# Kernel optimization log

Measured on AMD Instinct MI355X. Metric: run time of the kernel, lower is better.

## Reference

```python
import jax, jax.numpy as jnp
import numpy as np

B = 4096          # batch size (scaled up from source's 16)
INPUT_AXIS = 784
LATENT_DIM = 2


def _pdist(x):
    # pairwise euclidean distances in itertools.combinations order (row-major upper triangle)
    sq = jnp.sum(x * x, axis=1)                      # [B]
    d2 = sq[:, None] + sq[None, :] - 2.0 * (x @ x.T)  # [B,B]
    i, j = jnp.triu_indices(x.shape[0], k=1)
    return jnp.sqrt(jnp.maximum(d2[i, j], 0.0))       # [B*(B-1)/2]


def setup_inputs() -> dict:
    key = jax.random.key(0)
    ks = jax.random.split(key, 17)
    dims = [(400, 784), (200, 400), (50, 200), (2, 50),
            (50, 2), (200, 50), (400, 200), (784, 400)]
    names = ['fc1', 'fc1_1', 'fc1_2', 'fc2', 'fc3', 'fc3_1', 'fc3_2', 'fc4']
    inp = {'x': jax.random.uniform(ks[0], (B, 1, 28, 28), dtype=jnp.float32)}
    for idx, (nm, (o, i)) in enumerate(zip(names, dims)):
        bound = 1.0 / np.sqrt(i)
        inp[nm + '_w'] = jax.random.uniform(ks[1 + 2 * idx], (o, i), jnp.float32, -bound, bound)
        inp[nm + '_b'] = jax.random.uniform(ks[2 + 2 * idx], (o,), jnp.float32, -bound, bound)
    return inp


def reference(x, fc1_w, fc1_b, fc1_1_w, fc1_1_b, fc1_2_w, fc1_2_b, fc2_w, fc2_b,
              fc3_w, fc3_b, fc3_1_w, fc3_1_b, fc3_2_w, fc3_2_b, fc4_w, fc4_b):
    lin = lambda h, w, b: h @ w.T + b
    lrelu = jax.nn.leaky_relu  # default slope 0.01, matches F.leaky_relu
    x2 = x.reshape(-1, INPUT_AXIS)                       # [B,784]
    h = lrelu(lin(x2, fc1_w, fc1_b))
    h = lrelu(lin(h, fc1_1_w, fc1_1_b))
    h = lrelu(lin(h, fc1_2_w, fc1_2_b))                  # encoder out [B,50]
    z = lin(jnp.tanh(h), fc2_w, fc2_b)                   # [B,2]
    y = lrelu(lin(z, fc3_w, fc3_b))
    y = lrelu(lin(y, fc3_1_w, fc3_1_b))
    y = lrelu(lin(y, fc3_2_w, fc3_2_b))
    y = jax.nn.sigmoid(lin(y, fc4_w, fc4_b))             # [B,784]
    y_img = y.reshape(B, 1, 28, 28)
    in_diff = _pdist(x2)
    lat_diff = _pdist(z)
    out_diff = _pdist(y.reshape(B, INPUT_AXIS))
    return (y_img, in_diff, lat_diff, out_diff, z)
```

## Files before the change

kernel.cpp:

```cpp
#include <hip/hip_runtime.h>
#include <math.h>

#define NB 4096
#define DIMX 784

typedef __attribute__((ext_vector_type(8))) short bf16x8;
typedef __attribute__((ext_vector_type(4))) float f32x4;

__device__ __forceinline__ float lrelu_f(float v) { return v >= 0.f ? v : 0.01f * v; }

__device__ __forceinline__ void split1(float x, short& hi_s, short& lo_s) {
    unsigned u = __float_as_uint(x);
    unsigned hib = (u + 0x7FFFu + ((u >> 16) & 1u)) & 0xFFFF0000u;
    float hif = __uint_as_float(hib);
    float lo = x - hif;
    unsigned ul = __float_as_uint(lo);
    unsigned lob = (ul + 0x7FFFu + ((ul >> 16) & 1u)) >> 16;
    hi_s = (short)(hib >> 16);
    lo_s = (short)lob;
}

#define GLL(srcp, dstp) __builtin_amdgcn_global_load_lds( \
    (const __attribute__((address_space(1))) void*)(srcp), \
    (__attribute__((address_space(3))) void*)(dstp), 16, 0, 0)


__global__ __launch_bounds__(256) void prep_all(
    const float* __restrict__ w1, const float* __restrict__ w11,
    const float* __restrict__ w32, const float* __restrict__ w4,
    short* __restrict__ o1, short* __restrict__ o11,
    short* __restrict__ o32, short* __restrict__ o4,
    const float* __restrict__ X, short* __restrict__ Xs,
    float* __restrict__ sqx, float* __restrict__ sqy)
{
    const int bid = blockIdx.x;
    const int t = threadIdx.x;
    if (bid < 3920) {
        const float* W; short* O; int N, K, NP, KP, base;
        if (bid < 1600)      { W = w1;  O = o1;  N = 400; K = 784; NP = 512; KP = 800; base = 0; }
        else if (bid < 2016) { W = w11; O = o11; N = 200; K = 400; NP = 256; KP = 416; base = 1600; }
        else if (bid < 2464) { W = w32; O = o32; N = 400; K = 200; NP = 512; KP = 224; base = 2016; }
        else                 { W = w4;  O = o4;  N = 784; K = 400; NP = 896; KP = 416; base = 2464; }
        const int idx = (bid - base) * 256 + t;
        if (idx >= NP * KP) return;
        const int r = idx / KP, k = idx - r * KP;
        short hi = 0, lo = 0;
        if (r < N && k < K) split1(W[(size_t)r * K + k], hi, lo);
        O[(size_t)r * 2 * KP + k]      = hi;
        O[(size_t)r * 2 * KP + KP + k] = lo;
    } else {
        const int r = bid - 3920;
        float s = 0.f;
        if (t < 200) {
            const int k0 = t * 4;
            short h[4] = {0, 0, 0, 0}, l[4] = {0, 0, 0, 0};
            if (k0 < 784) {
                float4 v = *(const float4*)(X + (size_t)r * 784 + k0);
                split1(v.x, h[0], l[0]); split1(v.y, h[1], l[1]);
                split1(v.z, h[2], l[2]); split1(v.w, h[3], l[3]);
                s = v.x * v.x + v.y * v.y + v.z * v.z + v.w * v.w;
            }
            *(uint2*)&Xs[(size_t)r * 1600 + k0]       = *(const uint2*)h;
            *(uint2*)&Xs[(size_t)r * 1600 + 800 + k0] = *(const uint2*)l;
        }
        __shared__ float red[256];
        red[t] = s;
        __syncthreads();
        for (int off = 128; off > 0; off >>= 1) {
            if (t < off) red[t] += red[t + off];
            __syncthreads();
        }
        if (t == 0) { sqx[r] = red[0]; sqy[r] = 0.f; }
    }
}

template<int ACT, bool WF32, bool WSPLIT, bool WROWSQ>
__global__ __launch_bounds__(256) void gemm3_64(
    const short* __restrict__ As_g, const short* __restrict__ Ws_g,
    const float* __restrict__ bias, float* __restrict__ C,
    short* __restrict__ Cs, int N, int KPi, int nchunk, int KPo,
    float* __restrict__ sqy)
{
    __shared__ short L[2][12288];
    const int tid = threadIdx.x;
    const int w = tid >> 6, lane = tid & 63;
    const int wc = w;
    const int m0 = blockIdx.y * 64, n0 = blockIdx.x * 128;
    const int frow = lane & 15;
    const int fk_sw = (((lane >> 4) ^ ((lane >> 1) & 3))) * 8;
    const int srow = tid >> 2;
    const int scol_sw = (((tid & 3) ^ ((tid >> 3) & 3))) * 8;
    const int RS = 2 * KPi;
    const int ld0 = w * 512;

    const short* gA  = As_g + (size_t)(m0 + srow) * RS + scol_sw;
    const short* gB0 = Ws_g + (size_t)(n0 + srow) * RS + scol_sw;
    const short* gB1 = gB0 + (size_t)64 * RS;

    f32x4 acc[4][2] = {};

    auto stage = [&](int buf, int km) {
        GLL(gA  + km,       &L[buf][ld0]);
        GLL(gA  + KPi + km, &L[buf][2048 + ld0]);
        GLL(gB0 + km,       &L[buf][4096 + ld0]);
        GLL(gB1 + km,       &L[buf][6144 + ld0]);
        GLL(gB0 + KPi + km, &L[buf][8192 + ld0]);
        GLL(gB1 + KPi + km, &L[buf][10240 + ld0]);
    };

    stage(0, 0);
    asm volatile("s_waitcnt vmcnt(0)" ::: "memory");
    __builtin_amdgcn_s_barrier();
    int buf = 0;
    #pragma unroll 1
    for (int cc = 0; cc < nchunk; ++cc) {
        if (cc + 1 < nchunk) {
            stage(buf ^ 1, (cc + 1) * 32);
            asm volatile("s_waitcnt vmcnt(6)" ::: "memory");
        } else {
            asm volatile("s_waitcnt vmcnt(0)" ::: "memory");
        }
        __builtin_amdgcn_s_barrier();

        bf16x8 ah[4], al[4], bh[2], bl[2];
        #pragma unroll
        for (int m = 0; m < 4; ++m) {
            const int ro = (m * 16 + frow) * 32 + fk_sw;
            ah[m] = *(const bf16x8*)&L[buf][ro];
            al[m] = *(const bf16x8*)&L[buf][2048 + ro];
        }
        #pragma unroll
        for (int n = 0; n < 2; ++n) {
            const int ro = (wc * 32 + n * 16 + frow) * 32 + fk_sw;
            bh[n] = *(const bf16x8*)&L[buf][4096 + ro];
            bl[n] = *(const bf16x8*)&L[buf][8192 + ro];
        }
        __builtin_amdgcn_s_setprio(1);
        #pragma unroll
        for (int m = 0; m < 4; ++m)
            #pragma unroll
            for (int n = 0; n < 2; ++n) {
                acc[m][n] = __builtin_amdgcn_mfma_f32_16x16x32_bf16(ah[m], bh[n], acc[m][n], 0, 0, 0);
                acc[m][n] = __builtin_amdgcn_mfma_f32_16x16x32_bf16(ah[m], bl[n], acc[m][n], 0, 0, 0);
                acc[m][n] = __builtin_amdgcn_mfma_f32_16x16x32_bf16(al[m], bh[n], acc[m][n], 0, 0, 0);
            }
        __builtin_amdgcn_s_setprio(0);
        __builtin_amdgcn_s_barrier();
        buf ^= 1;
    }

    const int col0 = lane & 15;
    const int row4 = (lane >> 4) * 4;

    float* rowsum = (float*)&L[0][0];
    if (WROWSQ) {
        __syncthreads();
        if (tid < 64) rowsum[tid] = 0.f;
        __syncthreads();
    }

    #pragma unroll
    for (int m = 0; m < 4; ++m) {
        #pragma unroll
        for (int r = 0; r < 4; ++r) {
            const int gm = m0 + m * 16 + row4 + r;
            float vsq = 0.f;
            #pragma unroll
            for (int n = 0; n < 2; ++n) {
                const int gn = n0 + wc * 32 + n * 16 + col0;
                float v = 0.f;
                if (gn < N) {
                    v = acc[m][n][r] + bias[gn];
                    if (ACT == 1)      v = lrelu_f(v);
                    else if (ACT == 2) v = 1.f / (1.f + expf(-v));
                }
                if (WF32 && gn < N) C[(size_t)gm * N + gn] = v;
                if (WSPLIT && gn < KPo) {
                    short hi, lo; split1(v, hi, lo);
                    Cs[(size_t)gm * 2 * KPo + gn]       = hi;
                    Cs[(size_t)gm * 2 * KPo + KPo + gn] = lo;
                }
                if (WROWSQ) vsq = fmaf(v, v, vsq);
            }
            if (WROWSQ) atomicAdd(&rowsum[m * 16 + row4 + r], vsq);
        }
    }
    if (WROWSQ) {
        __syncthreads();
        if (tid < 64) atomicAdd(&sqy[m0 + tid], rowsum[tid]);
    }
}

__global__ __launch_bounds__(256) void fused_mid(
    const float* __restrict__ h2, const float* __restrict__ W12,
    const float* __restrict__ b12, const float* __restrict__ W2,
    const float* __restrict__ b2,  const float* __restrict__ W3,
    const float* __restrict__ b3,  const float* __restrict__ W31,
    const float* __restrict__ b31, float* __restrict__ z_out,
    short* __restrict__ y2s)
{
    __shared__ float wbuf[200 * 51];
    __shared__ float hl[16 * 201];
    __shared__ float h3l[16 * 51];
    __shared__ float y1l[16 * 51];
    __shared__ float zl[16 * 2];
    __shared__ float w2l[100], w3l[100];
    __shared__ float b12l[50], b2l[2], b3l[50], b31l[200];
    const int t = threadIdx.x;
    const int r0 = blockIdx.x * 16;

    for (int i = t; i < 50 * 200; i += 256) { int n = i / 200, k = i - n * 200; wbuf[n * 201 + k] = W12[i]; }
    for (int i = t; i < 16 * 200; i += 256) { int r = i / 200, k = i - r * 200; hl[r * 201 + k] = h2[(size_t)(r0 + r) * 200 + k]; }
    for (int i = t; i < 100; i += 256) { w2l[i] = W2[i]; w3l[i] = W3[i]; }
    if (t < 50)  { b12l[t] = b12[t]; b3l[t] = b3[t]; }
    if (t < 2)   b2l[t] = b2[t];
    if (t < 200) b31l[t] = b31[t];
    __syncthreads();

    for (int i = t; i < 16 * 50; i += 256) {
        int r = i / 50, n = i - r * 50;
        float s = b12l[n];
        #pragma unroll 4
        for (int k = 0; k < 200; ++k) s = fmaf(hl[r * 201 + k], wbuf[n * 201 + k], s);
        h3l[r * 51 + n] = tanhf(lrelu_f(s));
    }
    __syncthreads();

    if (t < 32) {
        int r = t >> 1, n = t & 1;
        float s = b2l[n];
        #pragma unroll
        for (int k = 0; k < 50; ++k) s = fmaf(h3l[r * 51 + k], w2l[n * 50 + k], s);
        zl[r * 2 + n] = s;
        z_out[(size_t)(r0 + r) * 2 + n] = s;
    }
    for (int i = t; i < 200 * 50; i += 256) { int n = i / 50, k = i - n * 50; wbuf[n * 51 + k] = W31[i]; }
    __syncthreads();

    for (int i = t; i < 16 * 50; i += 256) {
        int r = i / 50, n = i - r * 50;
        float s = fmaf(zl[r * 2], w3l[n * 2], fmaf(zl[r * 2 + 1], w3l[n * 2 + 1], b3l[n]));
        y1l[r * 51 + n] = lrelu_f(s);
    }
    __syncthreads();

    for (int i = t; i < 16 * 224; i += 256) {
        int r = i / 224, n = i - r * 224;
        float v = 0.f;
        if (n < 200) {
            float s = b31l[n];
            #pragma unroll
            for (int k = 0; k < 50; ++k) s = fmaf(y1l[r * 51 + k], wbuf[n * 51 + k], s);
            v = lrelu_f(s);
        }
        short hi, lo; split1(v, hi, lo);
        const size_t gm = r0 + r;
        y2s[gm * 448 + n]       = hi;
        y2s[gm * 448 + 224 + n] = lo;
    }
}

__global__ __launch_bounds__(256, 4) void pdist_all(
    const short* __restrict__ xs, const short* __restrict__ ys,
    const float* __restrict__ sqx, const float* __restrict__ sqy,
    const float* __restrict__ Z, float* __restrict__ in_diff,
    float* __restrict__ out_diff, float* __restrict__ lat_diff)
{
    __shared__ short L[4][4096];
    const int tid = threadIdx.x;
    const int orig = blockIdx.x;

    if (orig < 528) {
        const int b = (orig & 7) * 66 + (orig >> 3);
        int rem = b, ti = 0;
        while (rem >= 32 - ti) { rem -= 32 - ti; ++ti; }
        const int tj = ti + rem;

        const int w = tid >> 6, lane = tid & 63;
        const int wr = w >> 1, wc = w & 1;
        const int frow = lane & 15;
        const int fk_sw = (((lane >> 4) ^ ((lane >> 1) & 3))) * 8;
        const int srow = tid >> 2;
        const int scol_sw = (((tid & 3) ^ ((tid >> 3) & 3))) * 8;
        const int i0 = ti * 128, j0 = tj * 128;
        const int ld0 = w * 512;

        const short* gA = ys + (size_t)(i0 + srow) * 1600 + scol_sw;
        const short* gB = ys + (size_t)(j0 + srow) * 1600 + scol_sw;
        const size_t half = (size_t)64 * 1600;

        f32x4 acc[4][4] = {};

        #pragma unroll 1
        for (int cc = 0; cc < 25; ++cc) {
            const int km = cc * 32;
            __syncthreads();
            GLL(gA + km,       &L[0][ld0]);   GLL(gA + half + km,       &L[0][2048 + ld0]);
            GLL(gB + km,       &L[2][ld0]);   GLL(gB + half + km,       &L[2][2048 + ld0]);
            GLL(gA + 800 + km, &L[1][ld0]);   GLL(gA + half + 800 + km, &L[1][2048 + ld0]);
            GLL(gB + 800 + km, &L[3][ld0]);   GLL(gB + half + 800 + km, &L[3][2048 + ld0]);
            __syncthreads();

            bf16x8 ah[4], bh[4];
            #pragma unroll
            for (int m = 0; m < 4; ++m)
                ah[m] = *(const bf16x8*)&L[0][(wr * 64 + m * 16 + frow) * 32 + fk_sw];
            #pragma unroll
            for (int n = 0; n < 4; ++n)
                bh[n] = *(const bf16x8*)&L[2][(wc * 64 + n * 16 + frow) * 32 + fk_sw];
            __builtin_amdgcn_s_setprio(1);
            #pragma unroll
            for (int m = 0; m < 4; ++m)
                #pragma unroll
                for (int n = 0; n < 4; ++n)
                    acc[m][n] = __builtin_amdgcn_mfma_f32_16x16x32_bf16(ah[m], bh[n], acc[m][n], 0, 0, 0);

            bf16x8 al[4], bl[4];
            #pragma unroll
            for (int n = 0; n < 4; ++n)
                bl[n] = *(const bf16x8*)&L[3][(wc * 64 + n * 16 + frow) * 32 + fk_sw];
            #pragma unroll
            for (int m = 0; m < 4; ++m)
                #pragma unroll
                for (int n = 0; n < 4; ++n)
                    acc[m][n] = __builtin_amdgcn_mfma_f32_16x16x32_bf16(ah[m], bl[n], acc[m][n], 0, 0, 0);
            #pragma unroll
            for (int m = 0; m < 4; ++m)
                al[m] = *(const bf16x8*)&L[1][(wr * 64 + m * 16 + frow) * 32 + fk_sw];
            #pragma unroll
            for (int m = 0; m < 4; ++m)
                #pragma unroll
                for (int n = 0; n < 4; ++n)
                    acc[m][n] = __builtin_amdgcn_mfma_f32_16x16x32_bf16(al[m], bh[n], acc[m][n], 0, 0, 0);
            __builtin_amdgcn_s_setprio(0);
        }

        const int col0 = lane & 15;
        const int row4 = (lane >> 4) * 4;
        float sqj_v[4];
        #pragma unroll
        for (int n = 0; n < 4; ++n)
            sqj_v[n] = sqy[j0 + wc * 64 + n * 16 + col0];

        #pragma unroll
        for (int m = 0; m < 4; ++m) {
            #pragma unroll
            for (int r = 0; r < 4; ++r) {
                const int gi = i0 + wr * 64 + m * 16 + row4 + r;
                const float sqi = sqy[gi];
                const int rowbase = (gi * (2 * NB - 1 - gi)) / 2 - gi - 1;
                #pragma unroll
                for (int n = 0; n < 4; ++n) {
                    const int gj = j0 + wc * 64 + n * 16 + col0;
                    if (gj > gi) {
                        float d2 = sqi + sqj_v[n] - 2.f * acc[m][n][r];
                        out_diff[rowbase + gj] = sqrtf(fmaxf(d2, 0.f));
                    }
                }
            }
        }
    } else if (orig < 1056) {
        const int o = orig - 528;
        const int b = (o & 7) * 66 + (o >> 3);
        int rem = b, ti = 0;
        while (rem >= 32 - ti) { rem -= 32 - ti; ++ti; }
        const int tj = ti + rem;

        const int w = tid >> 6, lane = tid & 63;
        const int wr = w >> 1, wc = w & 1;
        const int frow = lane & 15;
        const int fk_sw = (((lane >> 4) ^ ((lane >> 1) & 3))) * 8;
        const int srow = tid >> 2;
        const int scol_sw = (((tid & 3) ^ ((tid >> 3) & 3))) * 8;
        const int i0 = ti * 128, j0 = tj * 128;
        const int ld0 = w * 512;

        const short* gA = xs + (size_t)(i0 + srow) * 1600 + scol_sw;
        const short* gB = xs + (size_t)(j0 + srow) * 1600 + scol_sw;
        const size_t half = (size_t)64 * 1600;

        f32x4 acc[4][4] = {};

        auto stage = [&](int buf, int km) {
            short* dA = buf ? &L[2][0] : &L[0][0];
            short* dB = buf ? &L[3][0] : &L[1][0];
            GLL(gA + km,        dA + ld0);   GLL(gA + half + km, dA + 2048 + ld0);
            GLL(gB + km,        dB + ld0);   GLL(gB + half + km, dB + 2048 + ld0);
        };

        stage(0, 0);
        asm volatile("s_waitcnt vmcnt(0)" ::: "memory");
        __builtin_amdgcn_s_barrier();
        int buf = 0;
        #pragma unroll 1
        for (int cc = 0; cc < 25; ++cc) {
            if (cc < 24) {
                stage(buf ^ 1, (cc + 1) * 32);
                asm volatile("s_waitcnt vmcnt(4)" ::: "memory");
            } else {
                asm volatile("s_waitcnt vmcnt(0)" ::: "memory");
            }
            __builtin_amdgcn_s_barrier();

            const short* SA = buf ? &L[2][0] : &L[0][0];
            const short* SB = buf ? &L[3][0] : &L[1][0];
            bf16x8 a[4], bb[4];
            #pragma unroll
            for (int m = 0; m < 4; ++m)
                a[m] = *(const bf16x8*)&SA[(wr * 64 + m * 16 + frow) * 32 + fk_sw];
            #pragma unroll
            for (int n = 0; n < 4; ++n)
                bb[n] = *(const bf16x8*)&SB[(wc * 64 + n * 16 + frow) * 32 + fk_sw];
            __builtin_amdgcn_s_setprio(1);
            #pragma unroll
            for (int m = 0; m < 4; ++m)
                #pragma unroll
                for (int n = 0; n < 4; ++n)
                    acc[m][n] = __builtin_amdgcn_mfma_f32_16x16x32_bf16(a[m], bb[n], acc[m][n], 0, 0, 0);
            __builtin_amdgcn_s_setprio(0);
            __builtin_amdgcn_s_barrier();
            buf ^= 1;
        }

        const int col0 = lane & 15;
        const int row4 = (lane >> 4) * 4;
        float sqj_v[4];
        #pragma unroll
        for (int n = 0; n < 4; ++n)
            sqj_v[n] = sqx[j0 + wc * 64 + n * 16 + col0];
        #pragma unroll
        for (int m = 0; m < 4; ++m) {
            #pragma unroll
            for (int r = 0; r < 4; ++r) {
                const int gi = i0 + wr * 64 + m * 16 + row4 + r;
                const float sqi = sqx[gi];
                const int rowbase = (gi * (2 * NB - 1 - gi)) / 2 - gi - 1;
                #pragma unroll
                for (int n = 0; n < 4; ++n) {
                    const int gj = j0 + wc * 64 + n * 16 + col0;
                    if (gj > gi) {
                        float d2 = sqi + sqj_v[n] - 2.f * acc[m][n][r];
                        in_diff[rowbase + gj] = sqrtf(fmaxf(d2, 0.f));
                    }
                }
            }
        }
    } else {
        const int o = orig - 1056;
        const int b = (o & 7) * 66 + (o >> 3);
        int rem = b, ti = 0;
        while (rem >= 32 - ti) { rem -= 32 - ti; ++ti; }
        const int tj = ti + rem;
        const int i0 = ti * 128, j0 = tj * 128;

        float* zi = (float*)&L[0][0];
        float* zj = (float*)&L[0][512];
        if (tid < 128) {
            *(float2*)&zi[tid * 2] = *(const float2*)&Z[(size_t)(i0 + tid) * 2];
        } else {
            const int r = tid - 128;
            *(float2*)&zj[r * 2] = *(const float2*)&Z[(size_t)(j0 + r) * 2];
        }
        __syncthreads();

        const int ty = tid >> 4;
        const int tx = tid & 15;
        #pragma unroll
        for (int ii = 0; ii < 8; ++ii) {
            const int li = ty * 8 + ii;
            const int gi = i0 + li;
            const int rowbase = (gi * (2 * NB - 1 - gi)) / 2 - gi - 1;
            const float zi0 = zi[li * 2], zi1 = zi[li * 2 + 1];
            #pragma unroll
            for (int jj = 0; jj < 8; ++jj) {
                const int lj = tx * 8 + jj;
                const int gj = j0 + lj;
                if (gj > gi) {
                    float d0 = zi0 - zj[lj * 2];
                    float d1 = zi1 - zj[lj * 2 + 1];
                    lat_diff[rowbase + gj] = sqrtf(fmaf(d0, d0, d1 * d1));
                }
            }
        }
    }
}

extern "C" void kernel_launch(void* const* d_in, const int* in_sizes, int n_in,
                              void* d_out, int out_size, void* d_ws, size_t ws_size,
                              hipStream_t stream)
{
    const float* x       = (const float*)d_in[0];
    const float* fc1_w   = (const float*)d_in[1];
    const float* fc1_b   = (const float*)d_in[2];
    const float* fc11_w  = (const float*)d_in[3];
    const float* fc11_b  = (const float*)d_in[4];
    const float* fc12_w  = (const float*)d_in[5];
    const float* fc12_b  = (const float*)d_in[6];
    const float* fc2_w   = (const float*)d_in[7];
    const float* fc2_b   = (const float*)d_in[8];
    const float* fc3_w   = (const float*)d_in[9];
    const float* fc3_b   = (const float*)d_in[10];
    const float* fc31_w  = (const float*)d_in[11];
    const float* fc31_b  = (const float*)d_in[12];
    const float* fc32_w  = (const float*)d_in[13];
    const float* fc32_b  = (const float*)d_in[14];
    const float* fc4_w   = (const float*)d_in[15];
    const float* fc4_b   = (const float*)d_in[16];

    float* out = (float*)d_out;
    float* y        = out;
    float* in_diff  = out + 3211264;
    float* lat_diff = out + 11597824;
    float* out_diff = out + 19984384;
    float* z        = out + 28370944;

    float* ws   = (float*)d_ws;
    float* h2   = ws;
    float* h3u  = h2  + (size_t)4096 * 200;
    float* y1u  = h3u + (size_t)4096 * 50;
    float* sqx  = y1u + (size_t)4096 * 50;
    float* sqy  = sqx + 4096;
    short* xs   = (short*)(sqy + 4096);
    short* ys   = xs  + (size_t)NB * 1600;
    short* w1s  = ys  + (size_t)NB * 1600;
    short* w11s = w1s  + (size_t)512 * 1600;
    short* w32s = w11s + (size_t)256 * 832;
    short* w4s  = w32s + (size_t)512 * 448;
    short* h1s  = w4s  + (size_t)896 * 832;
    short* y3s  = h1s;
    short* y2s  = h1s  + (size_t)4096 * 832;

    const dim3 blk(256);

    prep_all<<<dim3(8016), blk, 0, stream>>>(
        fc1_w, fc11_w, fc32_w, fc4_w, w1s, w11s, w32s, w4s, x, xs, sqx, sqy);
    gemm3_64<1, false, true, false><<<dim3(4, 64), blk, 0, stream>>>(
        xs, w1s, fc1_b, nullptr, h1s, 400, 800, 25, 416, nullptr);
    gemm3_64<1, true, false, false><<<dim3(2, 64), blk, 0, stream>>>(
        h1s, w11s, fc11_b, h2, nullptr, 200, 416, 13, 0, nullptr);
    fused_mid<<<dim3(256), blk, 0, stream>>>(
        h2, fc12_w, fc12_b, fc2_w, fc2_b, fc3_w, fc3_b, fc31_w, fc31_b, z, y2s);
    gemm3_64<1, false, true, false><<<dim3(4, 64), blk, 0, stream>>>(
        y2s, w32s, fc32_b, nullptr, y3s, 400, 224, 7, 416, nullptr);
    gemm3_64<2, true, true, true><<<dim3(7, 64), blk, 0, stream>>>(
        y3s, w4s, fc4_b, y, ys, 784, 416, 13, 800, sqy);
    pdist_all<<<dim3(1584), blk, 0, stream>>>(
        xs, ys, sqx, sqy, z, in_diff, out_diff, lat_diff);
}
```

Baseline: 225.8 us.

## Compute output pairwise distances from bf16 high parts only, sharing the input-distance path

The fc4 GEMM now writes only the bf16 high half of y, with an 800-wide row stride, when HIONLY is set. The out_diff pairwise-distance tiles reuse the single-pass path already used for in_diff, replacing the three-pass hi/lo split-bf16 MFMA path. Row squared norms for both x and y are now computed from the rounded high parts, so they match the bf16 dot products. This cuts MFMA work and memory traffic for the output distances to about a third, at the cost of lower precision in out_diff.

```diff
diff --git a/kernel.cpp b/kernel.cpp
--- a/kernel.cpp
+++ b/kernel.cpp
@@ -9,7 +9,7 @@
 
 __device__ __forceinline__ float lrelu_f(float v) { return v >= 0.f ? v : 0.01f * v; }
 
-__device__ __forceinline__ void split1(float x, short& hi_s, short& lo_s) {
+__device__ __forceinline__ float split1h(float x, short& hi_s, short& lo_s) {
     unsigned u = __float_as_uint(x);
     unsigned hib = (u + 0x7FFFu + ((u >> 16) & 1u)) & 0xFFFF0000u;
     float hif = __uint_as_float(hib);
@@ -18,6 +18,7 @@
     unsigned lob = (ul + 0x7FFFu + ((ul >> 16) & 1u)) >> 16;
     hi_s = (short)(hib >> 16);
     lo_s = (short)lob;
+    return hif;
 }
 
 #define GLL(srcp, dstp) __builtin_amdgcn_global_load_lds( \
@@ -45,7 +46,7 @@
         if (idx >= NP * KP) return;
         const int r = idx / KP, k = idx - r * KP;
         short hi = 0, lo = 0;
-        if (r < N && k < K) split1(W[(size_t)r * K + k], hi, lo);
+        if (r < N && k < K) split1h(W[(size_t)r * K + k], hi, lo);
         O[(size_t)r * 2 * KP + k]      = hi;
         O[(size_t)r * 2 * KP + KP + k] = lo;
     } else {
@@ -56,9 +57,11 @@
             short h[4] = {0, 0, 0, 0}, l[4] = {0, 0, 0, 0};
             if (k0 < 784) {
                 float4 v = *(const float4*)(X + (size_t)r * 784 + k0);
-                split1(v.x, h[0], l[0]); split1(v.y, h[1], l[1]);
-                split1(v.z, h[2], l[2]); split1(v.w, h[3], l[3]);
-                s = v.x * v.x + v.y * v.y + v.z * v.z + v.w * v.w;
+                float h0 = split1h(v.x, h[0], l[0]);
+                float h1 = split1h(v.y, h[1], l[1]);
+                float h2v = split1h(v.z, h[2], l[2]);
+                float h3v = split1h(v.w, h[3], l[3]);
+                s = h0 * h0 + h1 * h1 + h2v * h2v + h3v * h3v;
             }
             *(uint2*)&Xs[(size_t)r * 1600 + k0]       = *(const uint2*)h;
             *(uint2*)&Xs[(size_t)r * 1600 + 800 + k0] = *(const uint2*)l;
@@ -74,7 +77,7 @@
     }
 }
 
-template<int ACT, bool WF32, bool WSPLIT, bool WROWSQ>
+template<int ACT, bool WF32, bool WSPLIT, bool WROWSQ, bool HIONLY>
 __global__ __launch_bounds__(256) void gemm3_64(
     const short* __restrict__ As_g, const short* __restrict__ Ws_g,
     const float* __restrict__ bias, float* __restrict__ C,
@@ -176,11 +179,16 @@
                 }
                 if (WF32 && gn < N) C[(size_t)gm * N + gn] = v;
                 if (WSPLIT && gn < KPo) {
-                    short hi, lo; split1(v, hi, lo);
-                    Cs[(size_t)gm * 2 * KPo + gn]       = hi;
-                    Cs[(size_t)gm * 2 * KPo + KPo + gn] = lo;
+                    short hi, lo;
+                    float hif = split1h(v, hi, lo);
+                    if (HIONLY) {
+                        Cs[(size_t)gm * KPo + gn] = hi;
+                    } else {
+                        Cs[(size_t)gm * 2 * KPo + gn]       = hi;
+                        Cs[(size_t)gm * 2 * KPo + KPo + gn] = lo;
+                    }
+                    if (WROWSQ) vsq = fmaf(hif, hif, vsq);
                 }
-                if (WROWSQ) vsq = fmaf(v, v, vsq);
             }
             if (WROWSQ) atomicAdd(&rowsum[m * 16 + row4 + r], vsq);
         }
@@ -253,7 +261,8 @@
             for (int k = 0; k < 50; ++k) s = fmaf(y1l[r * 51 + k], wbuf[n * 51 + k], s);
             v = lrelu_f(s);
         }
-        short hi, lo; split1(v, hi, lo);
+        short hi, lo;
+        split1h(v, hi, lo);
         const size_t gm = r0 + r;
         y2s[gm * 448 + n]       = hi;
         y2s[gm * 448 + 224 + n] = lo;
@@ -270,11 +279,18 @@
     const int tid = threadIdx.x;
     const int orig = blockIdx.x;
 
-    if (orig < 528) {
-        const int b = (orig & 7) * 66 + (orig >> 3);
+    if (orig < 1056) {
+        const bool isY = (orig < 528);
+        const int o = isY ? orig : orig - 528;
+        const int b = (o & 7) * 66 + (o >> 3);
         int rem = b, ti = 0;
         while (rem >= 32 - ti) { rem -= 32 - ti; ++ti; }
         const int tj = ti + rem;
+
+        const short* Xs = isY ? ys : xs;
+        const int rs    = isY ? 800 : 1600;
+        const float* sq = isY ? sqy : sqx;
+        float* outp     = isY ? out_diff : in_diff;
 
         const int w = tid >> 6, lane = tid & 63;
         const int wr = w >> 1, wc = w & 1;
@@ -285,99 +301,9 @@
         const int i0 = ti * 128, j0 = tj * 128;
         const int ld0 = w * 512;
 
-        const short* gA = ys + (size_t)(i0 + srow) * 1600 + scol_sw;
-        const short* gB = ys + (size_t)(j0 + srow) * 1600 + scol_sw;
-        const size_t half = (size_t)64 * 1600;
-
-        f32x4 acc[4][4] = {};
-
-        #pragma unroll 1
-        for (int cc = 0; cc < 25; ++cc) {
-            const int km = cc * 32;
-            __syncthreads();
-            GLL(gA + km,       &L[0][ld0]);   GLL(gA + half + km,       &L[0][2048 + ld0]);
-            GLL(gB + km,       &L[2][ld0]);   GLL(gB + half + km,       &L[2][2048 + ld0]);
-            GLL(gA + 800 + km, &L[1][ld0]);   GLL(gA + half + 800 + km, &L[1][2048 + ld0]);
-            GLL(gB + 800 + km, &L[3][ld0]);   GLL(gB + half + 800 + km, &L[3][2048 + ld0]);
-            __syncthreads();
-
-            bf16x8 ah[4], bh[4];
-            #pragma unroll
-            for (int m = 0; m < 4; ++m)
-                ah[m] = *(const bf16x8*)&L[0][(wr * 64 + m * 16 + frow) * 32 + fk_sw];
-            #pragma unroll
-            for (int n = 0; n < 4; ++n)
-                bh[n] = *(const bf16x8*)&L[2][(wc * 64 + n * 16 + frow) * 32 + fk_sw];
-            __builtin_amdgcn_s_setprio(1);
-            #pragma unroll
-            for (int m = 0; m < 4; ++m)
-                #pragma unroll
-                for (int n = 0; n < 4; ++n)
-                    acc[m][n] = __builtin_amdgcn_mfma_f32_16x16x32_bf16(ah[m], bh[n], acc[m][n], 0, 0, 0);
-
-            bf16x8 al[4], bl[4];
-            #pragma unroll
-            for (int n = 0; n < 4; ++n)
-                bl[n] = *(const bf16x8*)&L[3][(wc * 64 + n * 16 + frow) * 32 + fk_sw];
-            #pragma unroll
-            for (int m = 0; m < 4; ++m)
-                #pragma unroll
-                for (int n = 0; n < 4; ++n)
-                    acc[m][n] = __builtin_amdgcn_mfma_f32_16x16x32_bf16(ah[m], bl[n], acc[m][n], 0, 0, 0);
-            #pragma unroll
-            for (int m = 0; m < 4; ++m)
-                al[m] = *(const bf16x8*)&L[1][(wr * 64 + m * 16 + frow) * 32 + fk_sw];
-            #pragma unroll
-            for (int m = 0; m < 4; ++m)
-                #pragma unroll
-                for (int n = 0; n < 4; ++n)
-                    acc[m][n] = __builtin_amdgcn_mfma_f32_16x16x32_bf16(al[m], bh[n], acc[m][n], 0, 0, 0);
-            __builtin_amdgcn_s_setprio(0);
-        }
-
-        const int col0 = lane & 15;
-        const int row4 = (lane >> 4) * 4;
-        float sqj_v[4];
-        #pragma unroll
-        for (int n = 0; n < 4; ++n)
-            sqj_v[n] = sqy[j0 + wc * 64 + n * 16 + col0];
-
-        #pragma unroll
-        for (int m = 0; m < 4; ++m) {
-            #pragma unroll
-            for (int r = 0; r < 4; ++r) {
-                const int gi = i0 + wr * 64 + m * 16 + row4 + r;
-                const float sqi = sqy[gi];
-                const int rowbase = (gi * (2 * NB - 1 - gi)) / 2 - gi - 1;
-                #pragma unroll
-                for (int n = 0; n < 4; ++n) {
-                    const int gj = j0 + wc * 64 + n * 16 + col0;
-                    if (gj > gi) {
-                        float d2 = sqi + sqj_v[n] - 2.f * acc[m][n][r];
-                        out_diff[rowbase + gj] = sqrtf(fmaxf(d2, 0.f));
-                    }
-                }
-            }
-        }
-    } else if (orig < 1056) {
-        const int o = orig - 528;
-        const int b = (o & 7) * 66 + (o >> 3);
-        int rem = b, ti = 0;
-        while (rem >= 32 - ti) { rem -= 32 - ti; ++ti; }
-        const int tj = ti + rem;
-
-        const int w = tid >> 6, lane = tid & 63;
-        const int wr = w >> 1, wc = w & 1;
-        const int frow = lane & 15;
-        const int fk_sw = (((lane >> 4) ^ ((lane >> 1) & 3))) * 8;
-        const int srow = tid >> 2;
-        const int scol_sw = (((tid & 3) ^ ((tid >> 3) & 3))) * 8;
-        const int i0 = ti * 128, j0 = tj * 128;
-        const int ld0 = w * 512;
-
-        const short* gA = xs + (size_t)(i0 + srow) * 1600 + scol_sw;
-        const short* gB = xs + (size_t)(j0 + srow) * 1600 + scol_sw;
-        const size_t half = (size_t)64 * 1600;
+        const short* gA = Xs + (size_t)(i0 + srow) * rs + scol_sw;
+        const short* gB = Xs + (size_t)(j0 + srow) * rs + scol_sw;
+        const size_t half = (size_t)64 * rs;
 
         f32x4 acc[4][4] = {};
 
@@ -427,20 +353,20 @@
         float sqj_v[4];
         #pragma unroll
         for (int n = 0; n < 4; ++n)
-            sqj_v[n] = sqx[j0 + wc * 64 + n * 16 + col0];
+            sqj_v[n] = sq[j0 + wc * 64 + n * 16 + col0];
         #pragma unroll
         for (int m = 0; m < 4; ++m) {
             #pragma unroll
             for (int r = 0; r < 4; ++r) {
                 const int gi = i0 + wr * 64 + m * 16 + row4 + r;
-                const float sqi = sqx[gi];
+                const float sqi = sq[gi];
                 const int rowbase = (gi * (2 * NB - 1 - gi)) / 2 - gi - 1;
                 #pragma unroll
                 for (int n = 0; n < 4; ++n) {
                     const int gj = j0 + wc * 64 + n * 16 + col0;
                     if (gj > gi) {
                         float d2 = sqi + sqj_v[n] - 2.f * acc[m][n][r];
-                        in_diff[rowbase + gj] = sqrtf(fmaxf(d2, 0.f));
+                        outp[rowbase + gj] = sqrtf(fmaxf(d2, 0.f));
                     }
                 }
             }
@@ -534,15 +460,15 @@
 
     prep_all<<<dim3(8016), blk, 0, stream>>>(
         fc1_w, fc11_w, fc32_w, fc4_w, w1s, w11s, w32s, w4s, x, xs, sqx, sqy);
-    gemm3_64<1, false, true, false><<<dim3(4, 64), blk, 0, stream>>>(
+    gemm3_64<1, false, true, false, false><<<dim3(4, 64), blk, 0, stream>>>(
         xs, w1s, fc1_b, nullptr, h1s, 400, 800, 25, 416, nullptr);
-    gemm3_64<1, true, false, false><<<dim3(2, 64), blk, 0, stream>>>(
+    gemm3_64<1, true, false, false, false><<<dim3(2, 64), blk, 0, stream>>>(
         h1s, w11s, fc11_b, h2, nullptr, 200, 416, 13, 0, nullptr);
     fused_mid<<<dim3(256), blk, 0, stream>>>(
         h2, fc12_w, fc12_b, fc2_w, fc2_b, fc3_w, fc3_b, fc31_w, fc31_b, z, y2s);
-    gemm3_64<1, false, true, false><<<dim3(4, 64), blk, 0, stream>>>(
+    gemm3_64<1, false, true, false, false><<<dim3(4, 64), blk, 0, stream>>>(
         y2s, w32s, fc32_b, nullptr, y3s, 400, 224, 7, 416, nullptr);
-    gemm3_64<2, true, true, true><<<dim3(7, 64), blk, 0, stream>>>(
+    gemm3_64<2, true, true, true, true><<<dim3(7, 64), blk, 0, stream>>>(
         y3s, w4s, fc4_b, y, ys, 784, 416, 13, 800, sqy);
     pdist_all<<<dim3(1584), blk, 0, stream>>>(
         xs, ys, sqx, sqy, z, in_diff, out_diff, lat_diff);
```

Result: faster. 209.2 us, median of 2 (-7.3%).
